# Kernel tuning notes

Hardware: AMD Instinct MI355X
Metric: run time of the kernel (lower is better)

The kernel has to match this reference:

```python
import jax, jax.numpy as jnp
import numpy as np

NUM_INPUTS = 1024
NUM_HIDDENS = 1024
SIGMA = 0.01


def setup_inputs() -> dict:
    key = jax.random.key(0)
    ks = jax.random.split(key, 7)
    d, h = NUM_INPUTS, NUM_HIDDENS
    w = lambda k, *s: jax.random.normal(k, s, dtype=jnp.float32) * SIGMA
    return {
        "inputs": jax.random.normal(ks[0], (512, 64, d), dtype=jnp.float32),
        "W_xz": w(ks[1], d, h), "W_hz": w(ks[2], h, h), "b_z": jnp.zeros(h, jnp.float32),
        "W_xr": w(ks[3], d, h), "W_hr": w(ks[4], h, h), "b_r": jnp.zeros(h, jnp.float32),
        "W_xh": w(ks[5], d, h), "W_hh": w(ks[6], h, h), "b_h": jnp.zeros(h, jnp.float32),
    }


def reference(inputs, W_xz, W_hz, b_z, W_xr, W_hr, b_r, W_xh, W_hh, b_h):
    T, B, _ = inputs.shape
    H0 = jnp.zeros((B, NUM_HIDDENS), dtype=inputs.dtype)
    # Precompute input projections for all timesteps in one big GEMM each.
    Xz = inputs @ W_xz + b_z  # [T, B, H]
    Xr = inputs @ W_xr + b_r
    Xh = inputs @ W_xh + b_h

    def step(H, xs):
        xz, xr, xh = xs
        Z = jax.nn.sigmoid(xz + H @ W_hz)
        R = jax.nn.sigmoid(xr + H @ W_hr)
        H_tilde = jnp.tanh(xh + (R * H) @ W_hh)
        H_new = Z * H + (1.0 - Z) * H_tilde
        return H_new, H_new

    H_final, outputs = jax.lax.scan(step, H0, (Xz, Xr, Xh))
    return outputs, H_final  # outputs: [T, B, H] (stacked list), H_final: [B, H]
```

## Files before the change

### kernel.cpp

```cpp
#include <hip/hip_runtime.h>
#include <hip/hip_bf16.h>

#define T_STEPS 512
#define BATCH   64
#define HID     1024
#define NWG     128
#define NSLOT   32
#define SLOT_SH (4 * 16 * 1024)

typedef __attribute__((ext_vector_type(8))) short short8;
typedef __attribute__((ext_vector_type(4))) float f32x4;
typedef __attribute__((ext_vector_type(4))) int  i32x4;

static __device__ __forceinline__ float b2f(unsigned short u){
  union { unsigned u; float f; } c; c.u = ((unsigned)u) << 16; return c.f;
}
static __device__ __forceinline__ unsigned short f2b(float f){
  union { float f; unsigned u; } c; c.f = f;
  unsigned r = c.u + 0x7fffu + ((c.u >> 16) & 1u);
  return (unsigned short)(r >> 16);
}
static __device__ __forceinline__ float sigm(float x){ return 1.0f / (1.0f + __expf(-x)); }
static __device__ __forceinline__ float tanh_fast(float x){ return 2.0f / (1.0f + __expf(-2.0f * x)) - 1.0f; }

#define MFMA __builtin_amdgcn_mfma_f32_16x16x32_bf16

__global__ void gru_init_k(int* __restrict__ flags){
  int i = blockIdx.x * blockDim.x + threadIdx.x;
  if (i < 4 * 32 * 32)
    __hip_atomic_store(flags + i, 0, __ATOMIC_RELAXED, __HIP_MEMORY_SCOPE_AGENT);
}

__global__ void gru_prepw_k(const float* __restrict__ w0, const float* __restrict__ w1,
                            const float* __restrict__ w2, const float* __restrict__ w3,
                            const float* __restrict__ w4, const float* __restrict__ w5,
                            unsigned short* __restrict__ wt){
  __shared__ float tile[32][33];
  const float* src;
  switch (blockIdx.z){
    case 0: src = w0; break; case 1: src = w1; break; case 2: src = w2; break;
    case 3: src = w3; break; case 4: src = w4; break; default: src = w5; break;
  }
  int tx = threadIdx.x, ty = threadIdx.y;
  int x0 = blockIdx.x * 32, y0 = blockIdx.y * 32;
  #pragma unroll
  for (int i = 0; i < 32; i += 8)
    tile[ty + i][tx] = src[(size_t)(y0 + ty + i) * HID + x0 + tx];
  __syncthreads();
  unsigned short* dst = wt + (size_t)blockIdx.z * HID * HID;
  #pragma unroll
  for (int i = 0; i < 32; i += 8)
    dst[(size_t)(x0 + ty + i) * HID + y0 + tx] = f2b(tile[tx][ty + i]);
}

__global__ __launch_bounds__(512, 1) void gru_xproj_k(
    const float* __restrict__ inp,
    const unsigned short* __restrict__ wt,
    const float* __restrict__ bz, const float* __restrict__ br, const float* __restrict__ bh,
    unsigned short* __restrict__ G2)
{
  __shared__ __align__(16) unsigned short albs[32 * 1024];

  const int tid = threadIdx.x, wv = tid >> 6, lane = tid & 63;
  const int l16 = lane & 15, kq = lane >> 4;
  const int tt = blockIdx.x >> 1;
  const int rh = blockIdx.x & 1;
  const int rbase = rh * 32;
  const int g = blockIdx.y;
  const float* bias_p = (g == 0) ? bz : (g == 1) ? br : bh;

  char* sb = (char*)albs;
  const float* abase = inp + ((size_t)tt * 64 + rbase) * HID;
  #pragma unroll
  for (int p = 0; p < 16; ++p){
    int e = (p * 512 + tid) * 4;
    float4 v = *(const float4*)(abase + e);
    ushort4 o;
    o.x = f2b(v.x); o.y = f2b(v.y); o.z = f2b(v.z); o.w = f2b(v.w);
    int b = e * 2;
    *(ushort4*)(sb + (b ^ (((b >> 11) & 7) << 4))) = o;
  }
  __syncthreads();

  const int n0 = wv * 128;
  const unsigned short* wslab = wt + (size_t)(2 * g) * HID * HID;
  const unsigned short* wcol[8];
  float bias[8];
  #pragma unroll
  for (int c = 0; c < 8; ++c){
    int n = n0 + c * 16 + l16;
    wcol[c] = wslab + (size_t)n * HID + kq * 8;
    bias[c] = bias_p[n];
  }

  f32x4 acc[2][8];
  #pragma unroll
  for (int r = 0; r < 2; ++r)
    #pragma unroll
    for (int c = 0; c < 8; ++c) acc[r][c] = (f32x4){0.f,0.f,0.f,0.f};

  const int asw = (l16 & 7) << 4;
  for (int kk = 0; kk < HID; kk += 32){
    short8 a0 = *(const short8*)(sb + ((l16 * 2048 + kk * 2 + kq * 16) ^ asw));
    short8 a1 = *(const short8*)(sb + (((16 + l16) * 2048 + kk * 2 + kq * 16) ^ asw));
    #pragma unroll
    for (int c = 0; c < 8; ++c){
      short8 bf = *(const short8*)(wcol[c] + kk);
      acc[0][c] = MFMA(a0, bf, acc[0][c], 0, 0, 0);
      acc[1][c] = MFMA(a1, bf, acc[1][c], 0, 0, 0);
    }
  }

  unsigned short* gout = G2 + (((size_t)tt * 3 + g) * 2 + rh) * 32768;
  #pragma unroll
  for (int c = 0; c < 8; ++c){
    int n = n0 + c * 16 + l16;
    #pragma unroll
    for (int r = 0; r < 2; ++r){
      unsigned lo = (unsigned)f2b(acc[r][c][0] + bias[c]) | ((unsigned)f2b(acc[r][c][1] + bias[c]) << 16);
      unsigned hi = (unsigned)f2b(acc[r][c][2] + bias[c]) | ((unsigned)f2b(acc[r][c][3] + bias[c]) << 16);
      *(unsigned long long*)&gout[(size_t)n * 32 + r * 16 + kq * 4] =
        (unsigned long long)lo | ((unsigned long long)hi << 32);
    }
  }
}

static __device__ __forceinline__ void waitflags32(const int* fgrp, int target){
  const int lane = threadIdx.x & 63;
  const int* p = fgrp + (lane & 31) * 32;
  const bool mine = lane < 32;
  for (;;){
    int v = mine ? __hip_atomic_load(p, __ATOMIC_RELAXED, __HIP_MEMORY_SCOPE_AGENT)
                 : 0x7fffffff;
    if (__all(v >= target)) return;
    __builtin_amdgcn_s_sleep(1);
  }
}

static __device__ __forceinline__ void stage_in(const unsigned short* __restrict__ src,
                                                unsigned short* __restrict__ stg, int tid){
  char* sb = (char*)stg;
  const char* sc = (const char*)src;
  #pragma unroll
  for (int c = 0; c < 4; ++c){
    const int b = tid * 16 + c * 8192;
    short8 v = __builtin_nontemporal_load((const short8*)(sc + b));
    *(short8*)(sb + (b ^ (((b >> 11) & 7) << 4))) = v;
  }
}

static __device__ __forceinline__ void pub16(unsigned short* dst, const unsigned short* lds_src){
  i32x4 v = *(const i32x4*)lds_src;
  asm volatile("global_store_dwordx4 %0, %1, off sc0 sc1" :: "v"(dst), "v"(v) : "memory");
}

__global__ __launch_bounds__(512, 1) void gru_scan_k(
    const unsigned short* __restrict__ G2,
    const unsigned short* __restrict__ wt,
    float* __restrict__ out,
    unsigned short* __restrict__ hb,
    unsigned short* __restrict__ rh,
    int* __restrict__ flags)
{
  __shared__ __align__(16) unsigned short stage[16 * 1024];
  __shared__ float zlds[16 * 33];
  __shared__ float hlds[16 * 33];
  __shared__ __align__(16) unsigned short ostage[512];

  const int bid = blockIdx.x;
  const int rg  = bid & 3;
  const int cs  = bid >> 2;
  const int tid  = threadIdx.x;
  const int w    = tid >> 6;
  const int lane = tid & 63;
  const int l16  = lane & 15;
  const int kq   = lane >> 4;

  const int myct = (w < 4) ? (w & 1) : ((w < 6) ? (w - 4) : 0);
  const int col  = cs * 32 + myct * 16 + l16;
  const int gA   = (w >> 1) & 1;
  const int erow0 = kq * 4;
  const int ecol  = myct * 16 + l16;

  short8 wreg[32];
  if (w < 6){
    const int slot = (w < 2) ? 1 : (w < 4) ? 3 : 5;
    const unsigned short* p = wt + (size_t)slot * HID * HID + (size_t)col * HID + kq * 8;
    #pragma unroll
    for (int i = 0; i < 32; ++i) wreg[i] = *(const short8*)(p + i * 32);
  }

  int* fgrp   = flags + rg * 32 * 32;
  int* myflag = fgrp + cs * 32;

  for (int i = tid; i < 16 * 33; i += 512) hlds[i] = 0.f;
  __syncthreads();

  const int asw = (l16 & 7) << 4;
  const int abase = l16 * 2048 + kq * 16;
  const int pidx = tid - 448;
  const int prow = pidx >> 2, pc8 = (pidx & 3) * 8;

  const size_t g2rh = (size_t)(rg >> 1) * 32768;
  const int    g2r  = (rg & 1) * 16 + erow0;

  for (int t = 0; t < T_STEPS; ++t){
    unsigned short* hb_w = hb + (size_t)(t & (NSLOT - 1)) * SLOT_SH + rg * 16384;
    unsigned short* rh_w = rh + (size_t)(t & (NSLOT - 1)) * SLOT_SH + rg * 16384;
    const unsigned short* hb_r = hb + (size_t)((t - 1) & (NSLOT - 1)) * SLOT_SH + rg * 16384;

    unsigned long long gx = 0;
    if (w < 6){
      const int gate = (w < 4) ? gA : 2;
      gx = *(const unsigned long long*)
           (G2 + ((size_t)t * 3 + gate) * 65536 + g2rh + (size_t)col * 32 + g2r);
    }

    if (t){
      if (w == 0) waitflags32(fgrp, 2 * t);
      __syncthreads();
      stage_in(hb_r, stage, tid);
      __syncthreads();
    }
    if (w < 4){
      f32x4 a0 = {0.f,0.f,0.f,0.f}, a1 = {0.f,0.f,0.f,0.f};
      if (t){
        const char* sb = (const char*)stage;
        #pragma unroll
        for (int i = 0; i < 32; i += 2){
          short8 f0 = *(const short8*)(sb + ((abase + i * 64) ^ asw));
          short8 f1 = *(const short8*)(sb + ((abase + i * 64 + 64) ^ asw));
          a0 = MFMA(f0, wreg[i],     a0, 0, 0, 0);
          a1 = MFMA(f1, wreg[i + 1], a1, 0, 0, 0);
        }
      }
      #pragma unroll
      for (int j = 0; j < 4; ++j){
        float g = sigm(a0[j] + a1[j] + b2f((unsigned short)(gx >> (16 * j))));
        if (w < 2) zlds[(erow0 + j) * 33 + ecol] = g;
        else       ostage[(erow0 + j) * 32 + ecol] =
                     f2b(g * hlds[(erow0 + j) * 33 + ecol]);
      }
    }
    __syncthreads();

    if (t){
      if (tid >= 448) pub16(rh_w + prow * 1024 + cs * 32 + pc8, &ostage[prow * 32 + pc8]);
      if (tid == 448){
        asm volatile("s_waitcnt vmcnt(0)" ::: "memory");
        __hip_atomic_store(myflag, 2 * t + 1, __ATOMIC_RELAXED, __HIP_MEMORY_SCOPE_AGENT);
      }
      if (w == 0) waitflags32(fgrp, 2 * t + 1);
      __syncthreads();
      stage_in(rh_w, stage, tid);
      __syncthreads();
    }

    float hn[4];
    if (w == 4 || w == 5){
      f32x4 a0 = {0.f,0.f,0.f,0.f}, a1 = {0.f,0.f,0.f,0.f};
      if (t){
        const char* sb = (const char*)stage;
        #pragma unroll
        for (int i = 0; i < 32; i += 2){
          short8 f0 = *(const short8*)(sb + ((abase + i * 64) ^ asw));
          short8 f1 = *(const short8*)(sb + ((abase + i * 64 + 64) ^ asw));
          a0 = MFMA(f0, wreg[i],     a0, 0, 0, 0);
          a1 = MFMA(f1, wreg[i + 1], a1, 0, 0, 0);
        }
      }
      #pragma unroll
      for (int j = 0; j < 4; ++j){
        int i33 = (erow0 + j) * 33 + ecol;
        float ht = tanh_fast(a0[j] + a1[j] + b2f((unsigned short)(gx >> (16 * j))));
        float z  = zlds[i33], hp = hlds[i33];
        hn[j] = z * hp + (1.0f - z) * ht;
        hlds[i33] = hn[j];
        ostage[(erow0 + j) * 32 + ecol] = f2b(hn[j]);
      }
    }
    __syncthreads();
    if (t < T_STEPS - 1){
      if (tid >= 448) pub16(hb_w + prow * 1024 + cs * 32 + pc8, &ostage[prow * 32 + pc8]);
      if (tid == 448){
        asm volatile("s_waitcnt vmcnt(0)" ::: "memory");
        __hip_atomic_store(myflag, 2 * t + 2, __ATOMIC_RELAXED, __HIP_MEMORY_SCOPE_AGENT);
      }
    }
    if (w == 4 || w == 5){
      #pragma unroll
      for (int j = 0; j < 4; ++j){
        __builtin_nontemporal_store(hn[j],
            &out[((size_t)t * BATCH + rg * 16 + erow0 + j) * HID + col]);
        if (t == T_STEPS - 1)
          __builtin_nontemporal_store(hn[j],
              &out[(size_t)T_STEPS * BATCH * HID + (size_t)(rg * 16 + erow0 + j) * HID + col]);
      }
    }
  }
}

extern "C" void kernel_launch(void* const* d_in, const int* in_sizes, int n_in,
                              void* d_out, int out_size, void* d_ws, size_t ws_size,
                              hipStream_t stream){
  const float* inputs = (const float*)d_in[0];
  const float* W_xz = (const float*)d_in[1];
  const float* W_hz = (const float*)d_in[2];
  const float* b_z  = (const float*)d_in[3];
  const float* W_xr = (const float*)d_in[4];
  const float* W_hr = (const float*)d_in[5];
  const float* b_r  = (const float*)d_in[6];
  const float* W_xh = (const float*)d_in[7];
  const float* W_hh = (const float*)d_in[8];
  const float* b_h  = (const float*)d_in[9];
  float* out = (float*)d_out;

  char* ws = (char*)d_ws;
  int*            flags = (int*)ws;
  unsigned short* hb    = (unsigned short*)(ws + 16384);
  unsigned short* rh    = (unsigned short*)(ws + 16384 + 4194304);
  unsigned short* wt    = (unsigned short*)(ws + 16384 + 8388608);
  unsigned short* G2    = (unsigned short*)(ws + 16384 + 8388608 + 12582912);

  gru_init_k<<<16, 256, 0, stream>>>(flags);
  gru_prepw_k<<<dim3(32, 32, 6), dim3(32, 8), 0, stream>>>(W_xz, W_hz, W_xr, W_hr, W_xh, W_hh, wt);
  gru_xproj_k<<<dim3(1024, 3), 512, 0, stream>>>(inputs, wt, b_z, b_r, b_h, G2);
  gru_scan_k<<<NWG, 512, 0, stream>>>(G2, wt, out, hb, rh, flags);
}
```

Baseline: 3.756 ms.

## Fuse input projection into persistent scan kernel with producer blocks and ready flags

Merges the separate input-projection GEMM kernel into the scan kernel. 128 extra workgroups compute projection tiles in timestep order and signal per-timestep ready counters, while the 128 scan workgroups wait on those counters before loading gate inputs. The aim is to hide the projection work behind the latency-bound recurrence and save a kernel boundary, at the cost of relying on co-residency of all blocks and possible scan stalls or memory contention from the producers.

Result: faster. 3.019 ms, median of 2 (-19.6%).

```diff
diff --git a/kernel.cpp b/kernel.cpp
--- a/kernel.cpp
+++ b/kernel.cpp
@@ -4,7 +4,7 @@
 #define T_STEPS 512
 #define BATCH   64
 #define HID     1024
-#define NWG     128
+#define NBLK    256
 #define NSLOT   32
 #define SLOT_SH (4 * 16 * 1024)
 
@@ -25,10 +25,12 @@
 
 #define MFMA __builtin_amdgcn_mfma_f32_16x16x32_bf16
 
-__global__ void gru_init_k(int* __restrict__ flags){
+__global__ void gru_init_k(int* __restrict__ flags, int* __restrict__ gready){
   int i = blockIdx.x * blockDim.x + threadIdx.x;
   if (i < 4 * 32 * 32)
     __hip_atomic_store(flags + i, 0, __ATOMIC_RELAXED, __HIP_MEMORY_SCOPE_AGENT);
+  if (i < T_STEPS * 32)
+    __hip_atomic_store(gready + i, 0, __ATOMIC_RELAXED, __HIP_MEMORY_SCOPE_AGENT);
 }
 
 __global__ void gru_prepw_k(const float* __restrict__ w0, const float* __restrict__ w1,
@@ -53,78 +55,6 @@
     dst[(size_t)(x0 + ty + i) * HID + y0 + tx] = f2b(tile[tx][ty + i]);
 }
 
-__global__ __launch_bounds__(512, 1) void gru_xproj_k(
-    const float* __restrict__ inp,
-    const unsigned short* __restrict__ wt,
-    const float* __restrict__ bz, const float* __restrict__ br, const float* __restrict__ bh,
-    unsigned short* __restrict__ G2)
-{
-  __shared__ __align__(16) unsigned short albs[32 * 1024];
-
-  const int tid = threadIdx.x, wv = tid >> 6, lane = tid & 63;
-  const int l16 = lane & 15, kq = lane >> 4;
-  const int tt = blockIdx.x >> 1;
-  const int rh = blockIdx.x & 1;
-  const int rbase = rh * 32;
-  const int g = blockIdx.y;
-  const float* bias_p = (g == 0) ? bz : (g == 1) ? br : bh;
-
-  char* sb = (char*)albs;
-  const float* abase = inp + ((size_t)tt * 64 + rbase) * HID;
-  #pragma unroll
-  for (int p = 0; p < 16; ++p){
-    int e = (p * 512 + tid) * 4;
-    float4 v = *(const float4*)(abase + e);
-    ushort4 o;
-    o.x = f2b(v.x); o.y = f2b(v.y); o.z = f2b(v.z); o.w = f2b(v.w);
-    int b = e * 2;
-    *(ushort4*)(sb + (b ^ (((b >> 11) & 7) << 4))) = o;
-  }
-  __syncthreads();
-
-  const int n0 = wv * 128;
-  const unsigned short* wslab = wt + (size_t)(2 * g) * HID * HID;
-  const unsigned short* wcol[8];
-  float bias[8];
-  #pragma unroll
-  for (int c = 0; c < 8; ++c){
-    int n = n0 + c * 16 + l16;
-    wcol[c] = wslab + (size_t)n * HID + kq * 8;
-    bias[c] = bias_p[n];
-  }
-
-  f32x4 acc[2][8];
-  #pragma unroll
-  for (int r = 0; r < 2; ++r)
-    #pragma unroll
-    for (int c = 0; c < 8; ++c) acc[r][c] = (f32x4){0.f,0.f,0.f,0.f};
-
-  const int asw = (l16 & 7) << 4;
-  for (int kk = 0; kk < HID; kk += 32){
-    short8 a0 = *(const short8*)(sb + ((l16 * 2048 + kk * 2 + kq * 16) ^ asw));
-    short8 a1 = *(const short8*)(sb + (((16 + l16) * 2048 + kk * 2 + kq * 16) ^ asw));
-    #pragma unroll
-    for (int c = 0; c < 8; ++c){
-      short8 bf = *(const short8*)(wcol[c] + kk);
-      acc[0][c] = MFMA(a0, bf, acc[0][c], 0, 0, 0);
-      acc[1][c] = MFMA(a1, bf, acc[1][c], 0, 0, 0);
-    }
-  }
-
-  unsigned short* gout = G2 + (((size_t)tt * 3 + g) * 2 + rh) * 32768;
-  #pragma unroll
-  for (int c = 0; c < 8; ++c){
-    int n = n0 + c * 16 + l16;
-    #pragma unroll
-    for (int r = 0; r < 2; ++r){
-      unsigned lo = (unsigned)f2b(acc[r][c][0] + bias[c]) | ((unsigned)f2b(acc[r][c][1] + bias[c]) << 16);
-      unsigned hi = (unsigned)f2b(acc[r][c][2] + bias[c]) | ((unsigned)f2b(acc[r][c][3] + bias[c]) << 16);
-      *(unsigned long long*)&gout[(size_t)n * 32 + r * 16 + kq * 4] =
-        (unsigned long long)lo | ((unsigned long long)hi << 32);
-    }
-  }
-}
-
 static __device__ __forceinline__ void waitflags32(const int* fgrp, int target){
   const int lane = threadIdx.x & 63;
   const int* p = fgrp + (lane & 31) * 32;
@@ -153,24 +83,103 @@
   i32x4 v = *(const i32x4*)lds_src;
   asm volatile("global_store_dwordx4 %0, %1, off sc0 sc1" :: "v"(dst), "v"(v) : "memory");
 }
-
-__global__ __launch_bounds__(512, 1) void gru_scan_k(
-    const unsigned short* __restrict__ G2,
+static __device__ __forceinline__ void pub8(unsigned short* dst, unsigned long long v){
+  asm volatile("global_store_dwordx2 %0, %1, off sc0 sc1" :: "v"(dst), "v"(v) : "memory");
+}
+
+__global__ __launch_bounds__(512, 1) void gru_main_k(
+    const float* __restrict__ inp,
     const unsigned short* __restrict__ wt,
+    const float* __restrict__ bz, const float* __restrict__ br, const float* __restrict__ bh,
+    unsigned short* __restrict__ G2,
     float* __restrict__ out,
     unsigned short* __restrict__ hb,
     unsigned short* __restrict__ rh,
-    int* __restrict__ flags)
+    int* __restrict__ flags,
+    int* __restrict__ gready)
 {
-  __shared__ __align__(16) unsigned short stage[16 * 1024];
-  __shared__ float zlds[16 * 33];
-  __shared__ float hlds[16 * 33];
-  __shared__ __align__(16) unsigned short ostage[512];
-
+  __shared__ __align__(16) char smem[98304];
   const int bid = blockIdx.x;
+  const int tid = threadIdx.x;
+
+  if (bid >= 128){
+    const int d = bid - 128;
+    const int wv = tid >> 6, lane = tid & 63;
+    const int l16 = lane & 15, kq = lane >> 4;
+    char* sb = (char*)smem;
+    const int asw = (l16 & 7) << 4;
+
+    for (int i = 0; i < 24; ++i){
+      const int tau = i * 128 + d;
+      const int tt = tau / 6, rem = tau % 6, g = rem >> 1, rhh = rem & 1;
+      const float* bias_p = (g == 0) ? bz : (g == 1) ? br : bh;
+
+      const float* abase = inp + ((size_t)tt * 64 + rhh * 32) * HID;
+      #pragma unroll
+      for (int p = 0; p < 16; ++p){
+        int e = (p * 512 + tid) * 4;
+        float4 v = *(const float4*)(abase + e);
+        ushort4 o;
+        o.x = f2b(v.x); o.y = f2b(v.y); o.z = f2b(v.z); o.w = f2b(v.w);
+        int b = e * 2;
+        *(ushort4*)(sb + (b ^ (((b >> 11) & 7) << 4))) = o;
+      }
+      __syncthreads();
+
+      const int n0 = wv * 128;
+      const unsigned short* wslab = wt + (size_t)(2 * g) * HID * HID;
+      const unsigned short* wcol[8];
+      float bias[8];
+      #pragma unroll
+      for (int c = 0; c < 8; ++c){
+        int n = n0 + c * 16 + l16;
+        wcol[c] = wslab + (size_t)n * HID + kq * 8;
+        bias[c] = bias_p[n];
+      }
+      f32x4 acc[2][8];
+      #pragma unroll
+      for (int r = 0; r < 2; ++r)
+        #pragma unroll
+        for (int c = 0; c < 8; ++c) acc[r][c] = (f32x4){0.f,0.f,0.f,0.f};
+
+      for (int kk = 0; kk < HID; kk += 32){
+        short8 a0 = *(const short8*)(sb + ((l16 * 2048 + kk * 2 + kq * 16) ^ asw));
+        short8 a1 = *(const short8*)(sb + (((16 + l16) * 2048 + kk * 2 + kq * 16) ^ asw));
+        #pragma unroll
+        for (int c = 0; c < 8; ++c){
+          short8 bf = *(const short8*)(wcol[c] + kk);
+          acc[0][c] = MFMA(a0, bf, acc[0][c], 0, 0, 0);
+          acc[1][c] = MFMA(a1, bf, acc[1][c], 0, 0, 0);
+        }
+      }
+
+      unsigned short* gout = G2 + (((size_t)tt * 3 + g) * 2 + rhh) * 32768;
+      #pragma unroll
+      for (int c = 0; c < 8; ++c){
+        int n = n0 + c * 16 + l16;
+        #pragma unroll
+        for (int r = 0; r < 2; ++r){
+          unsigned lo = (unsigned)f2b(acc[r][c][0] + bias[c]) | ((unsigned)f2b(acc[r][c][1] + bias[c]) << 16);
+          unsigned hi = (unsigned)f2b(acc[r][c][2] + bias[c]) | ((unsigned)f2b(acc[r][c][3] + bias[c]) << 16);
+          pub8(&gout[(size_t)n * 32 + r * 16 + kq * 4],
+               (unsigned long long)lo | ((unsigned long long)hi << 32));
+        }
+      }
+      asm volatile("s_waitcnt vmcnt(0)" ::: "memory");
+      __syncthreads();
+      if (tid == 0)
+        __hip_atomic_fetch_add(gready + tt * 32, 1, __ATOMIC_RELAXED, __HIP_MEMORY_SCOPE_AGENT);
+    }
+    return;
+  }
+
+  unsigned short* stage  = (unsigned short*)smem;
+  float*          zlds   = (float*)(smem + 32768);
+  float*          hlds   = (float*)(smem + 34880);
+  unsigned short* ostage = (unsigned short*)(smem + 36992);
+
   const int rg  = bid & 3;
   const int cs  = bid >> 2;
-  const int tid  = threadIdx.x;
   const int w    = tid >> 6;
   const int lane = tid & 63;
   const int l16  = lane & 15;
@@ -211,9 +220,16 @@
 
     unsigned long long gx = 0;
     if (w < 6){
+      const int* gp = gready + t * 32;
+      int v = (lane == 0) ? __hip_atomic_load(gp, __ATOMIC_RELAXED, __HIP_MEMORY_SCOPE_AGENT) : 6;
+      while (!__all(v >= 6)){
+        __builtin_amdgcn_s_sleep(2);
+        v = (lane == 0) ? __hip_atomic_load(gp, __ATOMIC_RELAXED, __HIP_MEMORY_SCOPE_AGENT) : 6;
+      }
       const int gate = (w < 4) ? gA : 2;
-      gx = *(const unsigned long long*)
-           (G2 + ((size_t)t * 3 + gate) * 65536 + g2rh + (size_t)col * 32 + g2r);
+      gx = __hip_atomic_load((const unsigned long long*)
+             (G2 + ((size_t)t * 3 + gate) * 65536 + g2rh + (size_t)col * 32 + g2r),
+             __ATOMIC_RELAXED, __HIP_MEMORY_SCOPE_AGENT);
     }
 
     if (t){
@@ -316,14 +332,14 @@
   float* out = (float*)d_out;
 
   char* ws = (char*)d_ws;
-  int*            flags = (int*)ws;
-  unsigned short* hb    = (unsigned short*)(ws + 16384);
-  unsigned short* rh    = (unsigned short*)(ws + 16384 + 4194304);
-  unsigned short* wt    = (unsigned short*)(ws + 16384 + 8388608);
-  unsigned short* G2    = (unsigned short*)(ws + 16384 + 8388608 + 12582912);
-
-  gru_init_k<<<16, 256, 0, stream>>>(flags);
+  int*            flags  = (int*)ws;
+  int*            gready = (int*)(ws + 16384);
+  unsigned short* hb     = (unsigned short*)(ws + 81920);
+  unsigned short* rh     = (unsigned short*)(ws + 81920 + 4194304);
+  unsigned short* wt     = (unsigned short*)(ws + 81920 + 8388608);
+  unsigned short* G2     = (unsigned short*)(ws + 81920 + 8388608 + 12582912);
+
+  gru_init_k<<<64, 256, 0, stream>>>(flags, gready);
   gru_prepw_k<<<dim3(32, 32, 6), dim3(32, 8), 0, stream>>>(W_xz, W_hz, W_xr, W_hr, W_xh, W_hh, wt);
-  gru_xproj_k<<<dim3(1024, 3), 512, 0, stream>>>(inputs, wt, b_z, b_r, b_h, G2);
-  gru_scan_k<<<NWG, 512, 0, stream>>>(G2, wt, out, hb, rh, flags);
-}
+  gru_main_k<<<NBLK, 512, 0, stream>>>(inputs, wt, b_z, b_r, b_h, G2, out, hb, rh, flags, gready);
+}
```
